# Performance work log

Measured on AMD Instinct MI355X. Metric: run time of the kernel, lower is better.

The kernel has to match this reference:

```python
import jax, jax.numpy as jnp
import numpy as np
from jax import lax

SEQ, BATCH, IN, HID, LAYERS = 2048, 64, 256, 256, 2


def setup_inputs() -> dict:
    key = jax.random.key(0)
    ks = jax.random.split(key, 5)
    k = np.sqrt(1.0 / HID).astype(np.float32)  # torch uniform(-sqrt(1/hidden), sqrt(1/hidden))
    x = jax.random.normal(ks[0], (SEQ, BATCH, IN), dtype=jnp.float32)
    h_0 = jax.random.normal(ks[1], (LAYERS, BATCH, HID), dtype=jnp.float32)
    W = jax.random.uniform(ks[2], (LAYERS, HID, IN), minval=-k, maxval=k, dtype=jnp.float32)
    U = jax.random.uniform(ks[3], (LAYERS, HID, HID), minval=-k, maxval=k, dtype=jnp.float32)
    b = jax.random.uniform(ks[4], (LAYERS, HID), minval=-k, maxval=k, dtype=jnp.float32)
    return {"x": x, "h_0": h_0, "W": W, "U": U, "b": b}


def reference(x, h_0, W, U, b):
    # Each layer independently maps x[t] -> h[layer] (original code feeds x[t] to every layer).
    def step(h, x_t):
        # h: [L, B, H], x_t: [B, I]
        h_new = jnp.tanh(
            jnp.einsum('bi,lhi->lbh', x_t, W)
            + jnp.einsum('lbh,lgh->lbg', h, U)
            + b[:, None, :]
        )
        return h_new, h_new[-1]  # output collects last layer's state

    h_n, output = lax.scan(step, h_0, x)
    return output, h_n
```

## Files before the change

### kernel.cpp

```cpp
#include <hip/hip_runtime.h>
#include <math.h>

#define SEQ 2048
#define BATCH 64
#define INF 256
#define HID 256
#define NL 2

__global__ __launch_bounds__(256) void xw_kernel(
    const float* __restrict__ x,
    const float* __restrict__ W,
    const float* __restrict__ bias,
    float* __restrict__ pre0,
    float* __restrict__ pre1)
{
    __shared__ float As[64][68];
    __shared__ float Bs[64][68];

    const int mb = blockIdx.x * 64;
    const int nb = blockIdx.y * 64;
    const int l  = nb >> 8;
    const int hb = nb & 255;

    const int tid = threadIdx.x;
    const int tx = tid & 15;
    const int ty = tid >> 4;

    const float* Wl = W + (size_t)l * HID * INF;

    float acc[4][4] = {};

    const int lrow = tid >> 4;
    const int lkq  = tid & 15;

    for (int kb = 0; kb < INF; kb += 64) {
        #pragma unroll
        for (int rr = 0; rr < 4; ++rr) {
            const int m = lrow + rr * 16;
            float4 va = *(const float4*)&x[(size_t)(mb + m) * INF + kb + lkq * 4];
            As[lkq*4 + 0][m] = va.x; As[lkq*4 + 1][m] = va.y;
            As[lkq*4 + 2][m] = va.z; As[lkq*4 + 3][m] = va.w;
            float4 vb = *(const float4*)&Wl[(size_t)(hb + m) * INF + kb + lkq * 4];
            Bs[lkq*4 + 0][m] = vb.x; Bs[lkq*4 + 1][m] = vb.y;
            Bs[lkq*4 + 2][m] = vb.z; Bs[lkq*4 + 3][m] = vb.w;
        }
        __syncthreads();

        #pragma unroll 8
        for (int k = 0; k < 64; ++k) {
            float4 a = *(const float4*)&As[k][ty * 4];
            float4 b = *(const float4*)&Bs[k][tx * 4];
            acc[0][0] = fmaf(a.x, b.x, acc[0][0]);
            acc[0][1] = fmaf(a.x, b.y, acc[0][1]);
            acc[0][2] = fmaf(a.x, b.z, acc[0][2]);
            acc[0][3] = fmaf(a.x, b.w, acc[0][3]);
            acc[1][0] = fmaf(a.y, b.x, acc[1][0]);
            acc[1][1] = fmaf(a.y, b.y, acc[1][1]);
            acc[1][2] = fmaf(a.y, b.z, acc[1][2]);
            acc[1][3] = fmaf(a.y, b.w, acc[1][3]);
            acc[2][0] = fmaf(a.z, b.x, acc[2][0]);
            acc[2][1] = fmaf(a.z, b.y, acc[2][1]);
            acc[2][2] = fmaf(a.z, b.z, acc[2][2]);
            acc[2][3] = fmaf(a.z, b.w, acc[2][3]);
            acc[3][0] = fmaf(a.w, b.x, acc[3][0]);
            acc[3][1] = fmaf(a.w, b.y, acc[3][1]);
            acc[3][2] = fmaf(a.w, b.z, acc[3][2]);
            acc[3][3] = fmaf(a.w, b.w, acc[3][3]);
        }
        __syncthreads();
    }

    float bv[4];
    #pragma unroll
    for (int j = 0; j < 4; ++j)
        bv[j] = bias[l * HID + hb + tx * 4 + j];

    float* dst = (l == 0) ? pre0 : pre1;
    #pragma unroll
    for (int i = 0; i < 4; ++i) {
        float4 o;
        o.x = acc[i][0] + bv[0];
        o.y = acc[i][1] + bv[1];
        o.z = acc[i][2] + bv[2];
        o.w = acc[i][3] + bv[3];
        *(float4*)&dst[(size_t)(mb + ty * 4 + i) * HID + hb + tx * 4] = o;
    }
}

__device__ __forceinline__ float tanh_fast(float x) {
    float xc = fminf(fmaxf(x, -12.0f), 12.0f);
    float e  = __expf(2.0f * xc);
    return __fdividef(e - 1.0f, e + 1.0f);
}

__global__ __launch_bounds__(1024, 4) void rnn_kernel(
    const float* __restrict__ h0,
    const float* __restrict__ U,
    const float* pre0,
    const float* pre1,
    float* out,
    float* hn)
{
    __shared__ float h_lds[2][4][72];

    const int l = blockIdx.x >> 6;
    const int b = blockIdx.x & 63;
    const int tid = threadIdx.x;
    const int g = tid >> 2;
    const int c = tid & 3;

    float4 u4[16];
    const float* Urow = U + (size_t)l * HID * HID + (size_t)g * HID + c * 64;
    #pragma unroll
    for (int q = 0; q < 16; ++q)
        u4[q] = *(const float4*)&Urow[q * 4];

    if (tid < HID)
        h_lds[0][tid >> 6][tid & 63] = h0[(size_t)l * BATCH * HID + (size_t)b * HID + tid];
    __syncthreads();

    const float* pre = (l == 0) ? pre0 : pre1;
    const size_t bh = (size_t)b * HID + g;

    float preCur = pre[bh];
    float v = 0.0f;
    int cur = 0;

    for (int t = 0; t < SEQ; ++t) {
        float preNext = (t + 1 < SEQ) ? pre[(size_t)(t + 1) * BATCH * HID + bh] : 0.0f;

        float a0 = 0.f, a1 = 0.f, a2 = 0.f, a3 = 0.f;
        const float* hseg = &h_lds[cur][c][0];
        #pragma unroll
        for (int q = 0; q < 16; ++q) {
            float4 hv = *(const float4*)&hseg[q * 4];
            a0 = fmaf(u4[q].x, hv.x, a0);
            a1 = fmaf(u4[q].y, hv.y, a1);
            a2 = fmaf(u4[q].z, hv.z, a2);
            a3 = fmaf(u4[q].w, hv.w, a3);
        }
        float s = (a0 + a1) + (a2 + a3);
        s += __shfl_xor(s, 1);
        s += __shfl_xor(s, 2);

        v = tanh_fast(s + preCur);

        if (c == 0) {
            h_lds[cur ^ 1][g >> 6][g & 63] = v;
            if (l == 1)
                out[(size_t)t * BATCH * HID + bh] = v;
        }
        preCur = preNext;
        cur ^= 1;
        __syncthreads();
    }

    if (c == 0)
        hn[(size_t)l * BATCH * HID + bh] = v;
}

extern "C" void kernel_launch(void* const* d_in, const int* in_sizes, int n_in,
                              void* d_out, int out_size, void* d_ws, size_t ws_size,
                              hipStream_t stream) {
    const float* x  = (const float*)d_in[0];
    const float* h0 = (const float*)d_in[1];
    const float* W  = (const float*)d_in[2];
    const float* U  = (const float*)d_in[3];
    const float* bs = (const float*)d_in[4];

    float* out  = (float*)d_out;
    float* pre0 = (float*)d_ws;
    float* pre1 = out;
    float* hn   = out + (size_t)SEQ * BATCH * HID;

    dim3 gridA(SEQ * BATCH / 64, (NL * HID) / 64);
    xw_kernel<<<gridA, 256, 0, stream>>>(x, W, bs, pre0, pre1);

    rnn_kernel<<<NL * BATCH, 1024, 0, stream>>>(h0, U, pre0, pre1, out, hn);
}
```

Baseline: 2.212 ms.

## Store recurrent weights and hidden state as fp16, use packed dot2 with 512-thread blocks

Converts U and the hidden state to packed fp16 and uses v_dot2 fp32-accumulate instructions. Each hidden unit is now computed by 2 threads instead of 4, so blocks shrink to 512 threads and one shuffle-reduction step goes away. Halving the thread count and LDS traffic per step is meant to shorten the serial per-timestep latency of the recurrence. The cost is fp16 rounding of weights and state over 2048 steps, which may drift from the fp32 reference.

```diff
diff --git a/kernel.cpp b/kernel.cpp
--- a/kernel.cpp
+++ b/kernel.cpp
@@ -6,6 +6,8 @@
 #define INF 256
 #define HID 256
 #define NL 2
+
+typedef __attribute__((ext_vector_type(2))) _Float16 half2_t;
 
 __global__ __launch_bounds__(256) void xw_kernel(
     const float* __restrict__ x,
@@ -93,7 +95,28 @@
     return __fdividef(e - 1.0f, e + 1.0f);
 }
 
-__global__ __launch_bounds__(1024, 4) void rnn_kernel(
+__device__ __forceinline__ float dot2(unsigned ua, unsigned ub, float c) {
+#if __has_builtin(__builtin_amdgcn_fdot2)
+    return __builtin_amdgcn_fdot2(__builtin_bit_cast(half2_t, ua),
+                                  __builtin_bit_cast(half2_t, ub), c, false);
+#else
+    half2_t a = __builtin_bit_cast(half2_t, ua);
+    half2_t b = __builtin_bit_cast(half2_t, ub);
+    c = fmaf((float)a.x, (float)b.x, c);
+    return fmaf((float)a.y, (float)b.y, c);
+#endif
+}
+
+__device__ __forceinline__ unsigned pk16(float a, float b) {
+#if __has_builtin(__builtin_amdgcn_cvt_pkrtz)
+    return __builtin_bit_cast(unsigned, __builtin_amdgcn_cvt_pkrtz(a, b));
+#else
+    half2_t h; h.x = (_Float16)a; h.y = (_Float16)b;
+    return __builtin_bit_cast(unsigned, h);
+#endif
+}
+
+__global__ __launch_bounds__(512, 2) void rnn_kernel(
     const float* __restrict__ h0,
     const float* __restrict__ U,
     const float* pre0,
@@ -101,22 +124,33 @@
     float* out,
     float* hn)
 {
-    __shared__ float h_lds[2][4][72];
+    __shared__ alignas(16) unsigned h16[2][128];
 
     const int l = blockIdx.x >> 6;
     const int b = blockIdx.x & 63;
     const int tid = threadIdx.x;
-    const int g = tid >> 2;
-    const int c = tid & 3;
-
-    float4 u4[16];
-    const float* Urow = U + (size_t)l * HID * HID + (size_t)g * HID + c * 64;
-    #pragma unroll
-    for (int q = 0; q < 16; ++q)
-        u4[q] = *(const float4*)&Urow[q * 4];
-
-    if (tid < HID)
-        h_lds[0][tid >> 6][tid & 63] = h0[(size_t)l * BATCH * HID + (size_t)b * HID + tid];
+    const int g = tid >> 1;
+    const int c = tid & 1;
+
+    uint4 uu[16];
+    const float* Urow = U + (size_t)l * HID * HID + (size_t)g * HID + c * 128;
+    #pragma unroll
+    for (int r = 0; r < 16; ++r) {
+        float4 f0 = *(const float4*)&Urow[r * 8];
+        float4 f1 = *(const float4*)&Urow[r * 8 + 4];
+        uu[r].x = pk16(f0.x, f0.y);
+        uu[r].y = pk16(f0.z, f0.w);
+        uu[r].z = pk16(f1.x, f1.y);
+        uu[r].w = pk16(f1.z, f1.w);
+    }
+    #pragma unroll
+    for (int r = 0; r < 16; ++r)
+        asm volatile("" : "+v"(uu[r].x), "+v"(uu[r].y), "+v"(uu[r].z), "+v"(uu[r].w));
+
+    if (tid < 128) {
+        const float* h0p = h0 + (size_t)l * BATCH * HID + (size_t)b * HID;
+        h16[0][tid] = pk16(h0p[tid * 2], h0p[tid * 2 + 1]);
+    }
     __syncthreads();
 
     const float* pre = (l == 0) ? pre0 : pre1;
@@ -130,23 +164,24 @@
         float preNext = (t + 1 < SEQ) ? pre[(size_t)(t + 1) * BATCH * HID + bh] : 0.0f;
 
         float a0 = 0.f, a1 = 0.f, a2 = 0.f, a3 = 0.f;
-        const float* hseg = &h_lds[cur][c][0];
+        const uint4* hc = (const uint4*)&h16[cur][c * 64];
         #pragma unroll
-        for (int q = 0; q < 16; ++q) {
-            float4 hv = *(const float4*)&hseg[q * 4];
-            a0 = fmaf(u4[q].x, hv.x, a0);
-            a1 = fmaf(u4[q].y, hv.y, a1);
-            a2 = fmaf(u4[q].z, hv.z, a2);
-            a3 = fmaf(u4[q].w, hv.w, a3);
+        for (int r = 0; r < 16; ++r) {
+            uint4 w = hc[r];
+            a0 = dot2(w.x, uu[r].x, a0);
+            a1 = dot2(w.y, uu[r].y, a1);
+            a2 = dot2(w.z, uu[r].z, a2);
+            a3 = dot2(w.w, uu[r].w, a3);
         }
         float s = (a0 + a1) + (a2 + a3);
         s += __shfl_xor(s, 1);
-        s += __shfl_xor(s, 2);
 
         v = tanh_fast(s + preCur);
 
+        float vp = __shfl_xor(v, 2);
         if (c == 0) {
-            h_lds[cur ^ 1][g >> 6][g & 63] = v;
+            if ((g & 1) == 0)
+                h16[cur ^ 1][g >> 1] = pk16(v, vp);
             if (l == 1)
                 out[(size_t)t * BATCH * HID + bh] = v;
         }
@@ -176,5 +211,5 @@
     dim3 gridA(SEQ * BATCH / 64, (NL * HID) / 64);
     xw_kernel<<<gridA, 256, 0, stream>>>(x, W, bs, pre0, pre1);
 
-    rnn_kernel<<<NL * BATCH, 1024, 0, stream>>>(h0, U, pre0, pre1, out, hn);
-}
+    rnn_kernel<<<NL * BATCH, 512, 0, stream>>>(h0, U, pre0, pre1, out, hn);
+}
```

Measured after the change: 2.137 ms. -3.4%, faster.
